# Kernel tuning notes

Hardware: AMD Instinct MI355X
Metric: run time of the kernel (lower is better)

The kernel has to match this reference:

```python
import jax, jax.numpy as jnp
import numpy as np

B, C_H, C_L = 8, 128, 256
H_H, W_H = 64, 64
H_L, W_L = 128, 128
CS = 8
K = CS * CS  # 64 external keys (== inter_channels, matches hardcoded reatt dim)
EPS = 1e-5


def _bn(x, g, b, m, v):
    # inference-mode BatchNorm2d over channel dim 1
    scale = g / jnp.sqrt(v + EPS)
    return (x - m[None, :, None, None]) * scale[None, :, None, None] + b[None, :, None, None]


def setup_inputs() -> dict:
    key = jax.random.key(0)
    ks = jax.random.split(key, 13)
    return {
        "x_h": jax.random.normal(ks[0], (B, C_H, H_H, W_H), jnp.float32),
        "x_l": jax.random.normal(ks[1], (B, C_L, H_L, W_L), jnp.float32),
        "bn_h_gamma": jax.random.normal(ks[2], (C_H,), jnp.float32),
        "bn_h_beta": jax.random.normal(ks[3], (C_H,), jnp.float32),
        "bn_h_mean": jax.random.normal(ks[4], (C_H,), jnp.float32),
        "bn_h_var": jax.random.uniform(ks[5], (C_H,), jnp.float32),
        "kv_w": jax.random.normal(ks[6], (2 * C_L, C_H), jnp.float32) * 0.05,
        "kv_b": jax.random.normal(ks[7], (2 * C_L,), jnp.float32) * 0.05,
        "bn_l_gamma": jax.random.normal(ks[8], (C_L,), jnp.float32),
        "bn_l_beta": jax.random.normal(ks[9], (C_L,), jnp.float32),
        "bn_l_mean": jax.random.normal(ks[10], (C_L,), jnp.float32),
        "bn_l_var": jax.random.uniform(ks[11], (C_L,), jnp.float32),
        "reatt": jax.random.normal(ks[12], (1, K, 1, 1), jnp.float32) * 1e-5,
    }


def reference(x_h, x_l, bn_h_gamma, bn_h_beta, bn_h_mean, bn_h_var,
              kv_w, kv_b, bn_l_gamma, bn_l_beta, bn_l_mean, bn_l_var, reatt):
    # ---- cross_kv: BN -> AdaptiveMaxPool2d(8,8) -> 1x1 conv ----
    xh = _bn(x_h, bn_h_gamma, bn_h_beta, bn_h_mean, bn_h_var)
    # exact window max pool (H_H, W_H divisible by CS)
    p = xh.reshape(B, C_H, CS, H_H // CS, CS, W_H // CS).max(axis=(3, 5))  # [B,C_H,8,8]
    kv = jnp.einsum('bchw,oc->bohw', p, kv_w) + kv_b[None, :, None, None]  # [B,2*C_L,8,8]
    ck = kv[:, :C_L]   # [B,C_L,8,8]
    cv = kv[:, C_L:]   # [B,C_L,8,8]
    # cross_k: permute NHWC then flatten -> per-sample [K, C_L] key matrix
    ck = ck.transpose(0, 2, 3, 1).reshape(B, K, C_L)
    # cross_v: flatten spatial -> per-sample [C_L, K] value matrix
    cv = cv.reshape(B, C_L, K)

    # ---- ExternalAttention (use_cross_kv path) ----
    xl = _bn(x_l, bn_l_gamma, bn_l_beta, bn_l_mean, bn_l_var)
    # grouped 1x1 conv (groups=B) == per-sample projection onto K external keys
    attn = jnp.einsum('bchw,bkc->bkhw', xl, ck)          # [B,K,H_L,W_L]
    attn = attn + reatt                                   # broadcast [1,K,1,1]
    # _act_sn: scale by inter_channels^-0.5, softmax over the K key channels
    attn = jax.nn.softmax(attn * (K ** -0.5), axis=1)
    # grouped 1x1 conv with values: per-sample [C_L,K] @ [K,H*W]
    out = jnp.einsum('bkhw,bck->bchw', attn, cv)          # [B,C_L,H_L,W_L]
    return x_l + out
```

## Files before the change

kernel.cpp:

```cpp
#include <hip/hip_runtime.h>
#include <math.h>

#define B_     8
#define C_H_   128
#define C_L_   256
#define K_     64
#define NPIX_L 16384
#define EPS_   1e-5f

#define P_OFF     0
#define P_SZ      (B_*K_*C_H_)
#define B1_BYTE   (P_SZ*4)
#define B2_BYTE   (B1_BYTE + B_*K_*C_L_*2)
#define BIAS_BYTE (B2_BYTE + B_*K_*C_L_*2)

typedef short bf16x8 __attribute__((ext_vector_type(8)));
typedef float f32x4  __attribute__((ext_vector_type(4)));

__device__ inline unsigned short f2bf(float f) {
    unsigned int u = __float_as_uint(f);
    u += 0x7FFFu + ((u >> 16) & 1u);
    return (unsigned short)(u >> 16);
}
__device__ inline unsigned int pack2bf(float lo, float hi) {
    unsigned int ul = __float_as_uint(lo);
    unsigned int uh = __float_as_uint(hi);
    ul = (ul + (0x7FFFu + ((ul >> 16) & 1u))) >> 16;
    uh = (uh + (0x7FFFu + ((uh >> 16) & 1u))) & 0xFFFF0000u;
    return ul | uh;
}

#define MFMA16(a, b, c) __builtin_amdgcn_mfma_f32_16x16x32_bf16((a), (b), (c), 0, 0, 0)

#define GLOAD_LDS16(g, l) __builtin_amdgcn_global_load_lds( \
    (const __attribute__((address_space(1))) void*)(g), \
    (__attribute__((address_space(3))) void*)(l), 16, 0, 0)

__global__ __launch_bounds__(256) void pool_bn_kernel(
    const float* __restrict__ x_h,
    const float* __restrict__ g, const float* __restrict__ be,
    const float* __restrict__ mn, const float* __restrict__ vr,
    float* __restrict__ ws)
{
    const int t   = threadIdx.x;
    const int k   = t & 63;
    const int cl  = t >> 6;
    const int bid = blockIdx.x;
    const int b   = bid >> 5;
    const int c   = ((bid & 31) << 2) + cl;

    const float* plane = x_h + ((size_t)(b * C_H_ + c) << 12);
    const int ph = k >> 3, pw = k & 7;
    const float* p0 = plane + (ph * 8) * 64 + pw * 8;

    float mx = -INFINITY, mnv = INFINITY;
#pragma unroll
    for (int i = 0; i < 8; i++) {
        const float4 a  = *reinterpret_cast<const float4*>(p0 + i * 64);
        const float4 bq = *reinterpret_cast<const float4*>(p0 + i * 64 + 4);
        mx  = fmaxf(mx,  fmaxf(fmaxf(a.x, a.y),  fmaxf(a.z, a.w)));
        mx  = fmaxf(mx,  fmaxf(fmaxf(bq.x, bq.y), fmaxf(bq.z, bq.w)));
        mnv = fminf(mnv, fminf(fminf(a.x, a.y),  fminf(a.z, a.w)));
        mnv = fminf(mnv, fminf(fminf(bq.x, bq.y), fminf(bq.z, bq.w)));
    }
    const float sc  = g[c] * rsqrtf(vr[c] + EPS_);
    const float sel = (sc >= 0.f) ? mx : mnv;
    ws[P_OFF + (b * K_ + k) * C_H_ + c] = fmaf(sel - mn[c], sc, be[c]);
}

__global__ __launch_bounds__(256) void kv_kernel(
    const float* __restrict__ kv_w, const float* __restrict__ kv_b,
    const float* __restrict__ lg, const float* __restrict__ lb,
    const float* __restrict__ lm, const float* __restrict__ lv,
    const float* __restrict__ ratt,
    float* __restrict__ ws)
{
    __shared__ __align__(16) float plds[4 * 132];
    __shared__ float red[4][4];
    const int t    = threadIdx.x;
    const int lane = t & 63;
    const int wid  = t >> 6;
    const int bid  = blockIdx.x;
    const int b    = bid >> 5;
    const int kg   = (bid >> 1) & 15;
    const int oh   = bid & 1;

    if (t < 128) {
        const int px = t >> 5, u = t & 31;
        const float4 v = *reinterpret_cast<const float4*>(
            ws + P_OFF + (size_t)(b * K_ + kg * 4 + px) * C_H_ + u * 4);
        *reinterpret_cast<float4*>(plds + px * 132 + u * 4) = v;
    }
    __syncthreads();

    const int oi = t >> 2;
    const int q4 = t & 3;
    const int kk = kg * 4 + q4;

    unsigned short* b1 = (unsigned short*)((char*)ws + B1_BYTE);
    unsigned short* b2 = (unsigned short*)((char*)ws + B2_BYTE);

    float bc = 0.f;
#pragma unroll
    for (int pass = 0; pass < 4; pass++) {
        const int o = oh * 256 + pass * 64 + oi;
        const float* wrow = kv_w + (size_t)o * C_H_ + q4 * 4;
        float a0 = 0.f, a1 = 0.f, a2 = 0.f, a3 = 0.f;
#pragma unroll
        for (int i = 0; i < 8; i++) {
            const float4 wf = *reinterpret_cast<const float4*>(wrow + i * 16);
            const float4 p0 = *reinterpret_cast<const float4*>(plds + 0 * 132 + i * 16 + q4 * 4);
            const float4 p1 = *reinterpret_cast<const float4*>(plds + 1 * 132 + i * 16 + q4 * 4);
            const float4 p2 = *reinterpret_cast<const float4*>(plds + 2 * 132 + i * 16 + q4 * 4);
            const float4 p3 = *reinterpret_cast<const float4*>(plds + 3 * 132 + i * 16 + q4 * 4);
            a0 = fmaf(wf.x, p0.x, a0); a0 = fmaf(wf.y, p0.y, a0);
            a0 = fmaf(wf.z, p0.z, a0); a0 = fmaf(wf.w, p0.w, a0);
            a1 = fmaf(wf.x, p1.x, a1); a1 = fmaf(wf.y, p1.y, a1);
            a1 = fmaf(wf.z, p1.z, a1); a1 = fmaf(wf.w, p1.w, a1);
            a2 = fmaf(wf.x, p2.x, a2); a2 = fmaf(wf.y, p2.y, a2);
            a2 = fmaf(wf.z, p2.z, a2); a2 = fmaf(wf.w, p2.w, a2);
            a3 = fmaf(wf.x, p3.x, a3); a3 = fmaf(wf.y, p3.y, a3);
            a3 = fmaf(wf.z, p3.z, a3); a3 = fmaf(wf.w, p3.w, a3);
        }
        a0 += __shfl_xor(a0, 1, 64); a0 += __shfl_xor(a0, 2, 64);
        a1 += __shfl_xor(a1, 1, 64); a1 += __shfl_xor(a1, 2, 64);
        a2 += __shfl_xor(a2, 1, 64); a2 += __shfl_xor(a2, 2, 64);
        a3 += __shfl_xor(a3, 1, 64); a3 += __shfl_xor(a3, 2, 64);
        float val = (q4 == 0) ? a0 : (q4 == 1) ? a1 : (q4 == 2) ? a2 : a3;
        val += kv_b[o];

        if (oh == 0) {
            const float s = lg[o] * rsqrtf(lv[o] + EPS_);
            const float h = fmaf(-lm[o], s, lb[o]);
            bc = fmaf(h, val, bc);
            const int s1 = o >> 5, j = o & 7;
            const int l  = ((o >> 3) & 3) * 16 + (kk & 15);
            const int n  = kk >> 4;
            b1[((((b * 8 + s1) * 4 + n) * 64) + l) * 8 + j] = f2bf(val * s);
        } else {
            const int co = o - 256;
            const int s2 = kk >> 5, j2 = kk & 7;
            const int l2 = ((kk >> 3) & 3) * 16 + (co & 15);
            const int n2 = co >> 4;
            b2[((((b * 2 + s2) * 16 + n2) * 64) + l2) * 8 + j2] = f2bf(val);
        }
    }

    if (oh == 0) {
#pragma unroll
        for (int m = 4; m < 64; m <<= 1) bc += __shfl_xor(bc, m, 64);
        if (lane < 4) red[wid][lane] = bc;
        __syncthreads();
        if (t < 4) {
            const float sum = red[0][t] + red[1][t] + red[2][t] + red[3][t];
            const int kkf = kg * 4 + t;
            float* bia = (float*)((char*)ws + BIAS_BYTE);
            bia[b * K_ + kkf] = (sum + ratt[kkf]) * 0.125f;
        }
    }
}

__global__ __launch_bounds__(256, 4) void attn_mfma(
    const float* __restrict__ x_l,
    const float* __restrict__ ws_f,
    float* __restrict__ out)
{
    __shared__ __align__(16) char lds[33280];
    float* xbuf0 = (float*)lds;
    float* xbuf1 = (float*)(lds + 16384);
    unsigned short* wscr = (unsigned short*)lds;
    float* obuf = (float*)(lds + 16384);

    const int t    = threadIdx.x;
    const int lane = t & 63;
    const int wid  = t >> 6;
    const int bid  = blockIdx.x;
    const int b    = bid & 7;
    const int tile = bid >> 3;
    const int px0  = tile * 128;
    const int pxw  = wid * 32;
    const int r16  = lane & 15;
    const int q    = lane >> 4;

    const unsigned short* b1 = (const unsigned short*)((const char*)ws_f + B1_BYTE);
    const unsigned short* b2 = (const unsigned short*)((const char*)ws_f + B2_BYTE);
    const float* biasf = (const float*)((const char*)ws_f + BIAS_BYTE) + b * K_;
    const float* xb = x_l + (size_t)b * (C_L_ * NPIX_L);
    float* ob = out + (size_t)b * (C_L_ * NPIX_L);

    float bl[4];
#pragma unroll
    for (int n = 0; n < 4; n++) bl[n] = biasf[16 * n + r16];

    const int su = ((lane & 31) ^ (wid << 2)) << 2;
    const int sd = lane >> 5;
#define STAGE(bufp, s_) do { \
    _Pragma("unroll") \
    for (int i_ = 0; i_ < 4; i_++) { \
        const int cl_ = 8 * wid + 2 * i_; \
        const float* gp_ = xb + (size_t)(32 * (s_) + cl_ + sd) * NPIX_L + px0 + su; \
        GLOAD_LDS16(gp_, (bufp) + (size_t)cl_ * 128); \
    } \
} while (0)

    f32x4 acc1[2][4] = {};
    union ABu { bf16x8 v; unsigned int u[4]; };

    STAGE(xbuf0, 0);

    const int p0x = (pxw + r16) ^ (q << 4);
    const int p1x = (pxw + 16 + r16) ^ (q << 4);

#pragma unroll
    for (int s = 0; s < 8; s++) {
        float* xbf = (s & 1) ? xbuf1 : xbuf0;
        if (s < 7) {
            STAGE((s & 1) ? xbuf0 : xbuf1, s + 1);
            asm volatile("s_waitcnt vmcnt(4)" ::: "memory");
        } else {
            asm volatile("s_waitcnt vmcnt(0)" ::: "memory");
        }
        __builtin_amdgcn_s_barrier();

        ABu a0f, a1f;
#pragma unroll
        for (int jj = 0; jj < 4; jj++) {
            const float* row0 = xbf + (8 * q + 2 * jj) * 128;
            const float* row1 = xbf + (8 * q + 2 * jj + 1) * 128;
            a0f.u[jj] = pack2bf(row0[p0x], row1[p0x]);
            a1f.u[jj] = pack2bf(row0[p1x], row1[p1x]);
        }
        const bf16x8* bp = ((const bf16x8*)b1) + ((b * 8 + s) * 4) * 64 + lane;
#pragma unroll
        for (int n = 0; n < 4; n++) {
            const bf16x8 bfr = bp[n * 64];
            acc1[0][n] = MFMA16(a0f.v, bfr, acc1[0][n]);
            acc1[1][n] = MFMA16(a1f.v, bfr, acc1[1][n]);
        }
        __builtin_amdgcn_s_barrier();
    }

    unsigned short* wsb = wscr + wid * 1152;
    bf16x8 af[2][2];
#pragma unroll
    for (int m = 0; m < 2; m++) {
#pragma unroll
        for (int r = 0; r < 4; r++) {
            float e0 = fmaf(acc1[m][0][r], 0.125f, bl[0]);
            float e1 = fmaf(acc1[m][1][r], 0.125f, bl[1]);
            float e2 = fmaf(acc1[m][2][r], 0.125f, bl[2]);
            float e3 = fmaf(acc1[m][3][r], 0.125f, bl[3]);
            float mx = fmaxf(fmaxf(e0, e1), fmaxf(e2, e3));
#pragma unroll
            for (int msk = 1; msk < 16; msk <<= 1) mx = fmaxf(mx, __shfl_xor(mx, msk, 64));
            e0 = __expf(e0 - mx); e1 = __expf(e1 - mx);
            e2 = __expf(e2 - mx); e3 = __expf(e3 - mx);
            float sm = (e0 + e1) + (e2 + e3);
#pragma unroll
            for (int msk = 1; msk < 16; msk <<= 1) sm += __shfl_xor(sm, msk, 64);
            const float inv = 1.f / sm;
            unsigned short* wp = wsb + (q * 4 + r) * 72 + r16;
            wp[0]  = f2bf(e0 * inv);
            wp[16] = f2bf(e1 * inv);
            wp[32] = f2bf(e2 * inv);
            wp[48] = f2bf(e3 * inv);
        }
#pragma unroll
        for (int s2 = 0; s2 < 2; s2++)
            af[m][s2] = *(const bf16x8*)(wsb + r16 * 72 + 32 * s2 + q * 8);
        if (m == 0) asm volatile("s_waitcnt lgkmcnt(0)" ::: "memory");
    }

#pragma unroll
    for (int nc = 0; nc < 4; nc++) {
        f32x4 acc2[2][4] = {};
#pragma unroll
        for (int s2 = 0; s2 < 2; s2++) {
            const bf16x8* bp2 = ((const bf16x8*)b2) + ((b * 2 + s2) * 16 + nc * 4) * 64 + lane;
#pragma unroll
            for (int nn = 0; nn < 4; nn++) {
                const bf16x8 bfr = bp2[nn * 64];
                acc2[0][nn] = MFMA16(af[0][s2], bfr, acc2[0][nn]);
                acc2[1][nn] = MFMA16(af[1][s2], bfr, acc2[1][nn]);
            }
        }
#pragma unroll
        for (int h = 0; h < 2; h++) {
#pragma unroll
            for (int m = 0; m < 2; m++)
#pragma unroll
                for (int e = 0; e < 2; e++) {
                    float* dp = obuf + (16 * e + r16) * 132 + (pxw + 16 * m + 4 * q);
                    *(f32x4*)dp = acc2[m][2 * h + e];
                }
            asm volatile("s_waitcnt lgkmcnt(0)" ::: "memory");
            __builtin_amdgcn_s_barrier();
            const int cbase = 64 * nc + 32 * h;
#pragma unroll
            for (int u2 = 0; u2 < 4; u2++) {
                const int idx = t + 256 * u2;
                const int col = idx >> 5;
                const int un  = idx & 31;
                const float4 vv = *(const float4*)(obuf + col * 132 + un * 4);
                const size_t gbase = (size_t)(cbase + col) * NPIX_L + px0 + un * 4;
                const float4 xv4 = *(const float4*)(xb + gbase);
                float4 o;
                o.x = vv.x + xv4.x; o.y = vv.y + xv4.y;
                o.z = vv.z + xv4.z; o.w = vv.w + xv4.w;
                *(float4*)(ob + gbase) = o;
            }
            __builtin_amdgcn_s_barrier();
        }
    }
#undef STAGE
}

extern "C" void kernel_launch(void* const* d_in, const int* in_sizes, int n_in,
                              void* d_out, int out_size, void* d_ws, size_t ws_size,
                              hipStream_t stream) {
    const float* x_h  = (const float*)d_in[0];
    const float* x_l  = (const float*)d_in[1];
    const float* hg   = (const float*)d_in[2];
    const float* hb   = (const float*)d_in[3];
    const float* hm   = (const float*)d_in[4];
    const float* hv   = (const float*)d_in[5];
    const float* kvw  = (const float*)d_in[6];
    const float* kvb  = (const float*)d_in[7];
    const float* lg   = (const float*)d_in[8];
    const float* lb   = (const float*)d_in[9];
    const float* lm   = (const float*)d_in[10];
    const float* lv   = (const float*)d_in[11];
    const float* ratt = (const float*)d_in[12];
    float* ws  = (float*)d_ws;
    float* out = (float*)d_out;

    pool_bn_kernel<<<256, 256, 0, stream>>>(x_h, hg, hb, hm, hv, ws);
    kv_kernel<<<256, 256, 0, stream>>>(kvw, kvb, lg, lb, lm, lv, ratt, ws);
    attn_mfma<<<1024, 256, 0, stream>>>(x_l, ws, out);
}
```

Baseline: 302.7 us.

## Halve attention pixel tile to 64 and prefetch key fragments for higher occupancy

Each attention block now handles 64 pixels instead of 128, so LDS drops to about 18KB, launch bounds rise to 6 blocks per CU, and the grid doubles to 2048 blocks. Each wave computes one 16-pixel M tile instead of two, which roughly halves the accumulator registers. The key-matrix B fragments are now double-buffered in registers and loaded one stage ahead of the MFMAs. In exchange, each block re-reads the B1/B2 weight fragments for half as many pixels, the output store loop needs more barrier rounds, and MFMA work per load shrinks.

```diff
diff --git a/kernel.cpp b/kernel.cpp
--- a/kernel.cpp
+++ b/kernel.cpp
@@ -160,16 +160,16 @@
     }
 }
 
-__global__ __launch_bounds__(256, 4) void attn_mfma(
+__global__ __launch_bounds__(256, 6) void attn_mfma(
     const float* __restrict__ x_l,
     const float* __restrict__ ws_f,
     float* __restrict__ out)
 {
-    __shared__ __align__(16) char lds[33280];
+    __shared__ __align__(16) char lds[17920];
     float* xbuf0 = (float*)lds;
-    float* xbuf1 = (float*)(lds + 16384);
-    unsigned short* wscr = (unsigned short*)lds;
-    float* obuf = (float*)(lds + 16384);
+    float* xbuf1 = (float*)(lds + 8192);
+    float* obuf  = (float*)lds;
+    unsigned short* wscr = (unsigned short*)(lds + 8704);
 
     const int t    = threadIdx.x;
     const int lane = t & 63;
@@ -177,8 +177,7 @@
     const int bid  = blockIdx.x;
     const int b    = bid & 7;
     const int tile = bid >> 3;
-    const int px0  = tile * 128;
-    const int pxw  = wid * 32;
+    const int px0  = tile * 64;
     const int r16  = lane & 15;
     const int q    = lane >> 4;
 
@@ -192,125 +191,118 @@
 #pragma unroll
     for (int n = 0; n < 4; n++) bl[n] = biasf[16 * n + r16];
 
-    const int su = ((lane & 31) ^ (wid << 2)) << 2;
-    const int sd = lane >> 5;
+    const int sd = lane >> 4;
+    const int su = ((lane & 15) << 2) ^ ((wid & 1) << 4);
 #define STAGE(bufp, s_) do { \
     _Pragma("unroll") \
-    for (int i_ = 0; i_ < 4; i_++) { \
-        const int cl_ = 8 * wid + 2 * i_; \
+    for (int i_ = 0; i_ < 2; i_++) { \
+        const int cl_ = 8 * wid + 4 * i_; \
         const float* gp_ = xb + (size_t)(32 * (s_) + cl_ + sd) * NPIX_L + px0 + su; \
-        GLOAD_LDS16(gp_, (bufp) + (size_t)cl_ * 128); \
+        GLOAD_LDS16(gp_, (bufp) + (size_t)cl_ * 64); \
     } \
 } while (0)
 
-    f32x4 acc1[2][4] = {};
+    f32x4 acc1[4] = {};
     union ABu { bf16x8 v; unsigned int u[4]; };
+    bf16x8 bfr[2][4];
+    const bf16x8* bbase = ((const bf16x8*)b1) + (b * 8 * 4) * 64 + lane;
 
     STAGE(xbuf0, 0);
-
-    const int p0x = (pxw + r16) ^ (q << 4);
-    const int p1x = (pxw + 16 + r16) ^ (q << 4);
+#pragma unroll
+    for (int n = 0; n < 4; n++) bfr[0][n] = bbase[n * 64];
+
+    const int p0x = (wid * 16 + r16) ^ ((q & 1) << 4);
 
 #pragma unroll
     for (int s = 0; s < 8; s++) {
-        float* xbf = (s & 1) ? xbuf1 : xbuf0;
+        const int p = s & 1;
+        float* xbf = p ? xbuf1 : xbuf0;
         if (s < 7) {
-            STAGE((s & 1) ? xbuf0 : xbuf1, s + 1);
-            asm volatile("s_waitcnt vmcnt(4)" ::: "memory");
+            STAGE(p ? xbuf0 : xbuf1, s + 1);
+            asm volatile("s_waitcnt vmcnt(2)" ::: "memory");
         } else {
             asm volatile("s_waitcnt vmcnt(0)" ::: "memory");
         }
         __builtin_amdgcn_s_barrier();
 
-        ABu a0f, a1f;
+        if (s < 7) {
+#pragma unroll
+            for (int n = 0; n < 4; n++) bfr[p ^ 1][n] = bbase[((s + 1) * 4 + n) * 64];
+        }
+
+        ABu a0f;
 #pragma unroll
         for (int jj = 0; jj < 4; jj++) {
-            const float* row0 = xbf + (8 * q + 2 * jj) * 128;
-            const float* row1 = xbf + (8 * q + 2 * jj + 1) * 128;
-            a0f.u[jj] = pack2bf(row0[p0x], row1[p0x]);
-            a1f.u[jj] = pack2bf(row0[p1x], row1[p1x]);
-        }
-        const bf16x8* bp = ((const bf16x8*)b1) + ((b * 8 + s) * 4) * 64 + lane;
-#pragma unroll
-        for (int n = 0; n < 4; n++) {
-            const bf16x8 bfr = bp[n * 64];
-            acc1[0][n] = MFMA16(a0f.v, bfr, acc1[0][n]);
-            acc1[1][n] = MFMA16(a1f.v, bfr, acc1[1][n]);
-        }
+            const float* row0 = xbf + (8 * q + 2 * jj) * 64;
+            a0f.u[jj] = pack2bf(row0[p0x], row0[64 + p0x]);
+        }
+#pragma unroll
+        for (int n = 0; n < 4; n++) acc1[n] = MFMA16(a0f.v, bfr[p][n], acc1[n]);
         __builtin_amdgcn_s_barrier();
     }
 
     unsigned short* wsb = wscr + wid * 1152;
-    bf16x8 af[2][2];
-#pragma unroll
-    for (int m = 0; m < 2; m++) {
-#pragma unroll
-        for (int r = 0; r < 4; r++) {
-            float e0 = fmaf(acc1[m][0][r], 0.125f, bl[0]);
-            float e1 = fmaf(acc1[m][1][r], 0.125f, bl[1]);
-            float e2 = fmaf(acc1[m][2][r], 0.125f, bl[2]);
-            float e3 = fmaf(acc1[m][3][r], 0.125f, bl[3]);
-            float mx = fmaxf(fmaxf(e0, e1), fmaxf(e2, e3));
-#pragma unroll
-            for (int msk = 1; msk < 16; msk <<= 1) mx = fmaxf(mx, __shfl_xor(mx, msk, 64));
-            e0 = __expf(e0 - mx); e1 = __expf(e1 - mx);
-            e2 = __expf(e2 - mx); e3 = __expf(e3 - mx);
-            float sm = (e0 + e1) + (e2 + e3);
-#pragma unroll
-            for (int msk = 1; msk < 16; msk <<= 1) sm += __shfl_xor(sm, msk, 64);
-            const float inv = 1.f / sm;
-            unsigned short* wp = wsb + (q * 4 + r) * 72 + r16;
-            wp[0]  = f2bf(e0 * inv);
-            wp[16] = f2bf(e1 * inv);
-            wp[32] = f2bf(e2 * inv);
-            wp[48] = f2bf(e3 * inv);
-        }
-#pragma unroll
-        for (int s2 = 0; s2 < 2; s2++)
-            af[m][s2] = *(const bf16x8*)(wsb + r16 * 72 + 32 * s2 + q * 8);
-        if (m == 0) asm volatile("s_waitcnt lgkmcnt(0)" ::: "memory");
-    }
-
-#pragma unroll
-    for (int nc = 0; nc < 4; nc++) {
-        f32x4 acc2[2][4] = {};
+#pragma unroll
+    for (int r = 0; r < 4; r++) {
+        float e0 = fmaf(acc1[0][r], 0.125f, bl[0]);
+        float e1 = fmaf(acc1[1][r], 0.125f, bl[1]);
+        float e2 = fmaf(acc1[2][r], 0.125f, bl[2]);
+        float e3 = fmaf(acc1[3][r], 0.125f, bl[3]);
+        float mx = fmaxf(fmaxf(e0, e1), fmaxf(e2, e3));
+#pragma unroll
+        for (int msk = 1; msk < 16; msk <<= 1) mx = fmaxf(mx, __shfl_xor(mx, msk, 64));
+        e0 = __expf(e0 - mx); e1 = __expf(e1 - mx);
+        e2 = __expf(e2 - mx); e3 = __expf(e3 - mx);
+        float sm = (e0 + e1) + (e2 + e3);
+#pragma unroll
+        for (int msk = 1; msk < 16; msk <<= 1) sm += __shfl_xor(sm, msk, 64);
+        const float inv = 1.f / sm;
+        unsigned short* wp = wsb + (q * 4 + r) * 72 + r16;
+        wp[0]  = f2bf(e0 * inv);
+        wp[16] = f2bf(e1 * inv);
+        wp[32] = f2bf(e2 * inv);
+        wp[48] = f2bf(e3 * inv);
+    }
+
+    bf16x8 af[2];
+#pragma unroll
+    for (int s2 = 0; s2 < 2; s2++)
+        af[s2] = *(const bf16x8*)(wsb + r16 * 72 + 32 * s2 + q * 8);
+
+#pragma unroll
+    for (int nc = 0; nc < 8; nc++) {
+        f32x4 acc2[2] = {};
 #pragma unroll
         for (int s2 = 0; s2 < 2; s2++) {
-            const bf16x8* bp2 = ((const bf16x8*)b2) + ((b * 2 + s2) * 16 + nc * 4) * 64 + lane;
-#pragma unroll
-            for (int nn = 0; nn < 4; nn++) {
-                const bf16x8 bfr = bp2[nn * 64];
-                acc2[0][nn] = MFMA16(af[0][s2], bfr, acc2[0][nn]);
-                acc2[1][nn] = MFMA16(af[1][s2], bfr, acc2[1][nn]);
+            const bf16x8* bp2 = ((const bf16x8*)b2) + ((b * 2 + s2) * 16 + nc * 2) * 64 + lane;
+#pragma unroll
+            for (int nn = 0; nn < 2; nn++) {
+                const bf16x8 bfr2 = bp2[nn * 64];
+                acc2[nn] = MFMA16(af[s2], bfr2, acc2[nn]);
             }
         }
 #pragma unroll
-        for (int h = 0; h < 2; h++) {
-#pragma unroll
-            for (int m = 0; m < 2; m++)
-#pragma unroll
-                for (int e = 0; e < 2; e++) {
-                    float* dp = obuf + (16 * e + r16) * 132 + (pxw + 16 * m + 4 * q);
-                    *(f32x4*)dp = acc2[m][2 * h + e];
-                }
-            asm volatile("s_waitcnt lgkmcnt(0)" ::: "memory");
-            __builtin_amdgcn_s_barrier();
-            const int cbase = 64 * nc + 32 * h;
-#pragma unroll
-            for (int u2 = 0; u2 < 4; u2++) {
-                const int idx = t + 256 * u2;
-                const int col = idx >> 5;
-                const int un  = idx & 31;
-                const float4 vv = *(const float4*)(obuf + col * 132 + un * 4);
-                const size_t gbase = (size_t)(cbase + col) * NPIX_L + px0 + un * 4;
-                const float4 xv4 = *(const float4*)(xb + gbase);
-                float4 o;
-                o.x = vv.x + xv4.x; o.y = vv.y + xv4.y;
-                o.z = vv.z + xv4.z; o.w = vv.w + xv4.w;
-                *(float4*)(ob + gbase) = o;
-            }
-            __builtin_amdgcn_s_barrier();
-        }
+        for (int nn = 0; nn < 2; nn++) {
+            float* dp = obuf + (16 * nn + r16) * 68 + wid * 16 + 4 * q;
+            *(f32x4*)dp = acc2[nn];
+        }
+        asm volatile("s_waitcnt lgkmcnt(0)" ::: "memory");
+        __builtin_amdgcn_s_barrier();
+        const int cbase = nc * 32;
+#pragma unroll
+        for (int u2 = 0; u2 < 2; u2++) {
+            const int idx = t + 256 * u2;
+            const int col = idx >> 4;
+            const int un  = idx & 15;
+            const float4 vv = *(const float4*)(obuf + col * 68 + un * 4);
+            const size_t gbase = (size_t)(cbase + col) * NPIX_L + px0 + un * 4;
+            const float4 xv4 = *(const float4*)(xb + gbase);
+            float4 o;
+            o.x = vv.x + xv4.x; o.y = vv.y + xv4.y;
+            o.z = vv.z + xv4.z; o.w = vv.w + xv4.w;
+            *(float4*)(ob + gbase) = o;
+        }
+        __builtin_amdgcn_s_barrier();
     }
 #undef STAGE
 }
@@ -336,5 +328,5 @@
 
     pool_bn_kernel<<<256, 256, 0, stream>>>(x_h, hg, hb, hm, hv, ws);
     kv_kernel<<<256, 256, 0, stream>>>(kvw, kvb, lg, lb, lm, lv, ratt, ws);
-    attn_mfma<<<1024, 256, 0, stream>>>(x_l, ws, out);
-}
+    attn_mfma<<<2048, 256, 0, stream>>>(x_l, ws, out);
+}
```

Result: no change. 308.6 us (+2.0%).
